# Performance work log

Hardware: AMD Instinct MI355X
Metric: run time of the kernel (lower is better)

## Reference

```python
import jax, jax.numpy as jnp
import numpy as np
import math


def setup_inputs() -> dict:
    key = jax.random.key(0)
    kq, kk, kv, km = jax.random.split(key, 4)
    B, Lq, Lk, D = 4, 4096, 4096, 64
    queries = jax.random.normal(kq, (B, Lq, D), dtype=jnp.float32)
    keys = jax.random.normal(kk, (B, Lk, D), dtype=jnp.float32)
    values = jax.random.normal(kv, (B, Lk, D), dtype=jnp.float32)
    masks = jax.random.randint(km, (B, Lk), 0, 2, dtype=jnp.int32)
    return {"queries": queries, "keys": keys, "values": values, "masks": masks}


def reference(queries, keys, values, masks):
    # scale = sqrt(d_k) (self.scale is None)
    d_k = queries.shape[-1]
    scale = math.sqrt(d_k)
    # scores: [B, Lq, Lk]
    scores = jnp.einsum('bqd,bkd->bqk', queries, keys) / jnp.asarray(scale, queries.dtype)
    # key-padding mask [B, Lk] -> broadcast over Lq; masked positions -> -inf
    neg_inf = jnp.asarray(float('-inf'), scores.dtype)
    scores = jnp.where(masks[:, None, :] == 0, neg_inf, scores)
    attn = jax.nn.softmax(scores, axis=-1)  # dropout p=0 -> identity
    return jnp.einsum('bqk,bkd->bqd', attn, values)
```

## Files before the change

### kernel.cpp

```cpp
#include <hip/hip_runtime.h>


#define B_N    4
#define L      4096
#define DH     64
#define TILE_K 64
#define BLOCK_Q 64
#define KPAD   72
#define SPLIT  4
#define SLAB   (L / SPLIT)
#define TILES  (SLAB / TILE_K)
#define QSCALE 0.18033688f

typedef unsigned short ushort8_ma __attribute__((ext_vector_type(8), may_alias));
typedef unsigned short ushort4_ma __attribute__((ext_vector_type(4), may_alias));
typedef float          f32x4_ma   __attribute__((ext_vector_type(4), may_alias));
typedef short          short8     __attribute__((ext_vector_type(8)));
typedef float          f32x4      __attribute__((ext_vector_type(4)));

union v8cast { ushort8_ma u; short8 s; };

static __device__ __forceinline__ short8 ld8(const unsigned short* p) {
    v8cast x; x.u = *(const ushort8_ma*)p; return x.s;
}
static __device__ __forceinline__ unsigned short bf16rne(float f) {
    union { float f; unsigned u; } x; x.f = f;
    unsigned r = x.u + 0x7fffu + ((x.u >> 16) & 1u);
    return (unsigned short)(r >> 16);
}
static __device__ __forceinline__ float fast_exp2(float x) {
    return __builtin_amdgcn_exp2f(x);
}

__global__ __launch_bounds__(256)
void prepass2(const float* __restrict__ Q, const float* __restrict__ K,
              const float* __restrict__ V,
              unsigned short* __restrict__ Qb, unsigned short* __restrict__ Kb,
              unsigned short* __restrict__ Vt)
{
    __shared__ unsigned short t[64][68];
    const int b  = blockIdx.y;
    const int r0 = blockIdx.x * 64;
    const size_t base = ((size_t)b * L + r0) * DH;

    for (int i = threadIdx.x; i < 1024; i += 256) {
        int row = i >> 4, d0 = (i & 15) * 4;
        size_t off = base + (size_t)row * DH + d0;
        f32x4_ma q = *(const f32x4_ma*)(Q + off);
        f32x4_ma k = *(const f32x4_ma*)(K + off);
        f32x4_ma v = *(const f32x4_ma*)(V + off);
        ushort4_ma qo, ko;
        #pragma unroll
        for (int j = 0; j < 4; ++j) {
            qo[j] = bf16rne(q[j] * QSCALE);
            ko[j] = bf16rne(k[j]);
            t[d0 + j][row] = bf16rne(v[j]);
        }
        *(ushort4_ma*)(Qb + off) = qo;
        *(ushort4_ma*)(Kb + off) = ko;
    }
    __syncthreads();
    for (int i = threadIdx.x; i < 1024; i += 256) {
        int d = i >> 4, k4 = (i & 15) * 4;
        ushort4_ma vo = { t[d][k4], t[d][k4 + 1], t[d][k4 + 2], t[d][k4 + 3] };
        *(ushort4_ma*)(Vt + ((size_t)b * DH + d) * L + r0 + k4) = vo;
    }
}

__global__ __launch_bounds__(256)
void fa_split(const unsigned short* __restrict__ Qb,
              const unsigned short* __restrict__ Kb,
              const unsigned short* __restrict__ Vt,
              const int*            __restrict__ Mk,
              float* __restrict__ ACCp, float* __restrict__ Lp)
{
    __shared__ unsigned short Kl[TILE_K * KPAD];
    __shared__ unsigned short Vl[DH * KPAD];
    __shared__ unsigned short Pl[4][16 * KPAD];
    __shared__ int            Ml[TILE_K];

    const int tid  = threadIdx.x;
    const int wave = tid >> 6;
    const int lane = tid & 63;
    const int l16  = lane & 15;
    const int quad = lane >> 4;

    const int b      = blockIdx.y & (B_N - 1);
    const int slab   = blockIdx.y >> 2;
    const int qblock = blockIdx.x * BLOCK_Q;
    const int kbase  = slab * SLAB;

    short8 aQ[2];
    {
        const unsigned short* qp = Qb + ((size_t)b * L + qblock + wave * 16 + l16) * DH;
        #pragma unroll
        for (int kk = 0; kk < 2; ++kk)
            aQ[kk] = ld8(qp + kk * 32 + quad * 8);
    }

    const unsigned short* Kbb = Kb + (size_t)b * L * DH;
    const unsigned short* Vtb = Vt + (size_t)b * DH * L;
    const int*            Mb  = Mk + (size_t)b * L;

    const int c1 = tid + 256;
    const int r0 = tid >> 3, d0 = (tid & 7) * 8;
    const int r1 = c1 >> 3,  d1 = (c1 & 7) * 8;

    ushort8_ma kr0, kr1, vr0, vr1;
    int mr;

    kr0 = *(const ushort8_ma*)(Kbb + (size_t)(kbase + r0) * DH + d0);
    kr1 = *(const ushort8_ma*)(Kbb + (size_t)(kbase + r1) * DH + d1);
    vr0 = *(const ushort8_ma*)(Vtb + (size_t)r0 * L + kbase + d0);
    vr1 = *(const ushort8_ma*)(Vtb + (size_t)r1 * L + kbase + d1);
    mr  = Mb[kbase + lane];
    *(ushort8_ma*)(&Kl[r0 * KPAD + d0]) = kr0;
    *(ushort8_ma*)(&Kl[r1 * KPAD + d1]) = kr1;
    *(ushort8_ma*)(&Vl[r0 * KPAD + d0]) = vr0;
    *(ushort8_ma*)(&Vl[r1 * KPAD + d1]) = vr1;
    if (wave == 0) Ml[lane] = mr;
    __syncthreads();

    f32x4 acc_o[4];
    float rs[4] = {0.f, 0.f, 0.f, 0.f};
    const f32x4 zero4 = {0.f, 0.f, 0.f, 0.f};
    #pragma unroll
    for (int n = 0; n < 4; ++n) acc_o[n] = zero4;

    unsigned short* pw = &Pl[wave][0];

    for (int t = 0; t < TILES; ++t) {
        if (t < TILES - 1) {
            const int k0n = kbase + (t + 1) * TILE_K;
            kr0 = *(const ushort8_ma*)(Kbb + (size_t)(k0n + r0) * DH + d0);
            kr1 = *(const ushort8_ma*)(Kbb + (size_t)(k0n + r1) * DH + d1);
            vr0 = *(const ushort8_ma*)(Vtb + (size_t)r0 * L + k0n + d0);
            vr1 = *(const ushort8_ma*)(Vtb + (size_t)r1 * L + k0n + d1);
            mr  = Mb[k0n + lane];
        }

        f32x4 s[4];
        #pragma unroll
        for (int n = 0; n < 4; ++n) {
            f32x4 acc = zero4;
            #pragma unroll
            for (int kk = 0; kk < 2; ++kk) {
                short8 bK = ld8(&Kl[(n * 16 + l16) * KPAD + kk * 32 + quad * 8]);
                acc = __builtin_amdgcn_mfma_f32_16x16x32_bf16(aQ[kk], bK, acc, 0, 0, 0);
            }
            s[n] = acc;
        }

        float bias[4];
        #pragma unroll
        for (int n = 0; n < 4; ++n) bias[n] = (Ml[n * 16 + l16] == 0) ? -1e30f : 0.f;
        #pragma unroll
        for (int n = 0; n < 4; ++n)
            #pragma unroll
            for (int r = 0; r < 4; ++r) {
                float p = fast_exp2(s[n][r] + bias[n]);
                rs[r] += p;
                pw[(quad * 4 + r) * KPAD + n * 16 + l16] = bf16rne(p);
            }

        #pragma unroll
        for (int kk = 0; kk < 2; ++kk) {
            short8 aP = ld8(&pw[l16 * KPAD + kk * 32 + quad * 8]);
            #pragma unroll
            for (int n = 0; n < 4; ++n) {
                short8 bV = ld8(&Vl[(n * 16 + l16) * KPAD + kk * 32 + quad * 8]);
                acc_o[n] = __builtin_amdgcn_mfma_f32_16x16x32_bf16(aP, bV, acc_o[n], 0, 0, 0);
            }
        }

        __syncthreads();
        if (t < TILES - 1) {
            *(ushort8_ma*)(&Kl[r0 * KPAD + d0]) = kr0;
            *(ushort8_ma*)(&Kl[r1 * KPAD + d1]) = kr1;
            *(ushort8_ma*)(&Vl[r0 * KPAD + d0]) = vr0;
            *(ushort8_ma*)(&Vl[r1 * KPAD + d1]) = vr1;
            if (wave == 0) Ml[lane] = mr;
            __syncthreads();
        }
    }

    const size_t pbase = ((size_t)(slab * B_N + b)) * L;
    #pragma unroll
    for (int r = 0; r < 4; ++r) {
        float t0 = rs[r];
        t0 += __shfl_xor(t0, 1);
        t0 += __shfl_xor(t0, 2);
        t0 += __shfl_xor(t0, 4);
        t0 += __shfl_xor(t0, 8);
        int qrow = qblock + wave * 16 + quad * 4 + r;
        float* ap = ACCp + (pbase + qrow) * DH;
        #pragma unroll
        for (int n = 0; n < 4; ++n)
            ap[n * 16 + l16] = acc_o[n][r];
        if (l16 == 0) Lp[pbase + qrow] = t0;
    }
}

__global__ __launch_bounds__(256)
void fa_combine(const float* __restrict__ ACCp, const float* __restrict__ Lp,
                float* __restrict__ O)
{
    const int b    = blockIdx.y;
    const int qrow = blockIdx.x * 4 + (threadIdx.x >> 6);
    const int d    = threadIdx.x & 63;

    float lsum = 0.f, o = 0.f;
    #pragma unroll
    for (int s = 0; s < SPLIT; ++s) {
        lsum += Lp[((size_t)(s * B_N + b)) * L + qrow];
        o    += ACCp[(((size_t)(s * B_N + b)) * L + qrow) * DH + d];
    }
    O[((size_t)b * L + qrow) * DH + d] = o / fmaxf(lsum, 1e-20f);
}

#define TK  64
#define RW  4
#define RB  16
#define KST 67

__global__ __launch_bounds__(256)
void fa_scalar(const float* __restrict__ Q, const float* __restrict__ K,
               const float* __restrict__ V, const int* __restrict__ Mk,
               float* __restrict__ O)
{
    __shared__ float Kt[TK][KST];
    __shared__ float Vts[DH][KST];
    __shared__ float Qs[RB][DH];
    __shared__ float Ps[4][RW][TK];
    __shared__ float Bs[TK];

    const int tid = threadIdx.x, w = tid >> 6, lane = tid & 63;
    const int b = blockIdx.y, row0 = blockIdx.x * RB;

    for (int i = tid; i < RB * DH; i += 256) {
        int r = i >> 6, d = i & 63;
        Qs[r][d] = Q[((size_t)b * L + row0 + r) * DH + d];
    }
    float m[RW], l[RW], acc[RW];
    #pragma unroll
    for (int rr = 0; rr < RW; ++rr) { m[rr] = -1e30f; l[rr] = 0.f; acc[rr] = 0.f; }

    for (int k0 = 0; k0 < L; k0 += TK) {
        __syncthreads();
        for (int i = tid; i < TK * DH; i += 256) {
            int key = i >> 6, d = i & 63;
            Kt[key][d]  = K[((size_t)b * L + k0 + key) * DH + d];
            Vts[d][key] = V[((size_t)b * L + k0 + key) * DH + d];
        }
        if (tid < TK) Bs[tid] = (Mk[(size_t)b * L + k0 + tid] == 0) ? -1e30f : 0.f;
        __syncthreads();
        float s[RW];
        #pragma unroll
        for (int rr = 0; rr < RW; ++rr) s[rr] = 0.f;
        for (int d4 = 0; d4 < DH; d4 += 4) {
            float kv[4];
            #pragma unroll
            for (int j = 0; j < 4; ++j) kv[j] = Kt[lane][d4 + j];
            #pragma unroll
            for (int rr = 0; rr < RW; ++rr)
                #pragma unroll
                for (int j = 0; j < 4; ++j)
                    s[rr] += Qs[w * RW + rr][d4 + j] * kv[j];
        }
        float alpha[RW];
        #pragma unroll
        for (int rr = 0; rr < RW; ++rr) {
            float sv = s[rr] * 0.125f + Bs[lane];
            float t = sv;
            #pragma unroll
            for (int off = 1; off < 64; off <<= 1) t = fmaxf(t, __shfl_xor(t, off));
            float mnew = fmaxf(m[rr], t);
            alpha[rr] = __expf(fminf(m[rr] - mnew, 0.f));
            float p = __expf(fminf(sv - mnew, 0.f));
            Ps[w][rr][lane] = p;
            float su = p;
            #pragma unroll
            for (int off = 1; off < 64; off <<= 1) su += __shfl_xor(su, off);
            l[rr] = l[rr] * alpha[rr] + su;
            m[rr] = mnew;
        }
        __syncthreads();
        #pragma unroll
        for (int rr = 0; rr < RW; ++rr) acc[rr] *= alpha[rr];
        for (int k4 = 0; k4 < TK; k4 += 4) {
            float vv[4];
            #pragma unroll
            for (int j = 0; j < 4; ++j) vv[j] = Vts[lane][k4 + j];
            #pragma unroll
            for (int rr = 0; rr < RW; ++rr)
                #pragma unroll
                for (int j = 0; j < 4; ++j)
                    acc[rr] += Ps[w][rr][k4 + j] * vv[j];
        }
    }
    #pragma unroll
    for (int rr = 0; rr < RW; ++rr) {
        int row = row0 + w * RW + rr;
        O[((size_t)b * L + row) * DH + lane] = acc[rr] / fmaxf(l[rr], 1e-20f);
    }
}

extern "C" void kernel_launch(void* const* d_in, const int* in_sizes, int n_in,
                              void* d_out, int out_size, void* d_ws, size_t ws_size,
                              hipStream_t stream) {
    const float* Q = (const float*)d_in[0];
    const float* K = (const float*)d_in[1];
    const float* V = (const float*)d_in[2];
    const int*   M = (const int*)d_in[3];
    float*       O = (float*)d_out;

    const size_t elems     = (size_t)B_N * L * DH;
    const size_t bf16_need = elems * 2 * 3;
    const size_t acc_elems = (size_t)SPLIT * B_N * L * DH;
    const size_t ml_elems  = (size_t)SPLIT * B_N * L;
    const size_t full_need = bf16_need + (acc_elems + ml_elems) * 4;

    unsigned short* Qb = (unsigned short*)d_ws;
    unsigned short* Kb = Qb + elems;
    unsigned short* Vt = Kb + elems;

    if (ws_size >= full_need) {
        float* ACCp = (float*)(Vt + elems);
        float* Lp   = ACCp + acc_elems;

        prepass2<<<dim3(L / 64, B_N), dim3(256), 0, stream>>>(Q, K, V, Qb, Kb, Vt);
        fa_split<<<dim3(L / BLOCK_Q, B_N * SPLIT), dim3(256), 0, stream>>>(
            Qb, Kb, Vt, M, ACCp, Lp);
        fa_combine<<<dim3(L / 4, B_N), dim3(256), 0, stream>>>(ACCp, Lp, O);
    } else {
        fa_scalar<<<dim3(L / RB, B_N), dim3(256), 0, stream>>>(Q, K, V, M, O);
    }
}
```

Before: 115.9 us.

## Fuse split-K combine into attention kernel via last-block atomic counter

Removes the separate combine kernel launch. Each split block now bumps an atomic counter per query block, and the last of the SPLIT blocks to finish reads the partial accumulators and row sums, normalises them and writes the output. The counters are zeroed in the prepass kernel. The P-to-bf16 conversion also changes from round-to-nearest-even to a cheaper round-half-up. This saves a launch and some scheduling gaps, at the cost of threadfences, an atomic, and a serialized tail in the last block for each query tile.

```diff
diff --git a/kernel.cpp b/kernel.cpp
--- a/kernel.cpp
+++ b/kernel.cpp
@@ -6,6 +6,7 @@
 #define DH     64
 #define TILE_K 64
 #define BLOCK_Q 64
+#define NQB    (L / BLOCK_Q)
 #define KPAD   72
 #define SPLIT  4
 #define SLAB   (L / SPLIT)
@@ -28,6 +29,10 @@
     unsigned r = x.u + 0x7fffu + ((x.u >> 16) & 1u);
     return (unsigned short)(r >> 16);
 }
+static __device__ __forceinline__ unsigned short bf16fast(float f) {
+    union { float f; unsigned u; } x; x.f = f;
+    return (unsigned short)((x.u + 0x8000u) >> 16);
+}
 static __device__ __forceinline__ float fast_exp2(float x) {
     return __builtin_amdgcn_exp2f(x);
 }
@@ -36,12 +41,15 @@
 void prepass2(const float* __restrict__ Q, const float* __restrict__ K,
               const float* __restrict__ V,
               unsigned short* __restrict__ Qb, unsigned short* __restrict__ Kb,
-              unsigned short* __restrict__ Vt)
+              unsigned short* __restrict__ Vt, int* __restrict__ Cnt)
 {
     __shared__ unsigned short t[64][68];
     const int b  = blockIdx.y;
     const int r0 = blockIdx.x * 64;
     const size_t base = ((size_t)b * L + r0) * DH;
+
+    if (blockIdx.x == 0 && threadIdx.x < NQB)
+        Cnt[b * NQB + threadIdx.x] = 0;
 
     for (int i = threadIdx.x; i < 1024; i += 256) {
         int row = i >> 4, d0 = (i & 15) * 4;
@@ -72,12 +80,15 @@
               const unsigned short* __restrict__ Kb,
               const unsigned short* __restrict__ Vt,
               const int*            __restrict__ Mk,
-              float* __restrict__ ACCp, float* __restrict__ Lp)
+              float* __restrict__ ACCp, float* __restrict__ Lp,
+              int* __restrict__ Cnt, float* __restrict__ O)
 {
     __shared__ unsigned short Kl[TILE_K * KPAD];
     __shared__ unsigned short Vl[DH * KPAD];
     __shared__ unsigned short Pl[4][16 * KPAD];
     __shared__ int            Ml[TILE_K];
+    __shared__ float          Linv[BLOCK_Q];
+    __shared__ int            lastFlag;
 
     const int tid  = threadIdx.x;
     const int wave = tid >> 6;
@@ -87,7 +98,8 @@
 
     const int b      = blockIdx.y & (B_N - 1);
     const int slab   = blockIdx.y >> 2;
-    const int qblock = blockIdx.x * BLOCK_Q;
+    const int qx     = blockIdx.x;
+    const int qblock = qx * BLOCK_Q;
     const int kbase  = slab * SLAB;
 
     short8 aQ[2];
@@ -160,7 +172,7 @@
             for (int r = 0; r < 4; ++r) {
                 float p = fast_exp2(s[n][r] + bias[n]);
                 rs[r] += p;
-                pw[(quad * 4 + r) * KPAD + n * 16 + l16] = bf16rne(p);
+                pw[(quad * 4 + r) * KPAD + n * 16 + l16] = bf16fast(p);
             }
 
         #pragma unroll
@@ -199,23 +211,39 @@
             ap[n * 16 + l16] = acc_o[n][r];
         if (l16 == 0) Lp[pbase + qrow] = t0;
     }
-}
-
-__global__ __launch_bounds__(256)
-void fa_combine(const float* __restrict__ ACCp, const float* __restrict__ Lp,
-                float* __restrict__ O)
-{
-    const int b    = blockIdx.y;
-    const int qrow = blockIdx.x * 4 + (threadIdx.x >> 6);
-    const int d    = threadIdx.x & 63;
-
-    float lsum = 0.f, o = 0.f;
-    #pragma unroll
-    for (int s = 0; s < SPLIT; ++s) {
-        lsum += Lp[((size_t)(s * B_N + b)) * L + qrow];
-        o    += ACCp[(((size_t)(s * B_N + b)) * L + qrow) * DH + d];
-    }
-    O[((size_t)b * L + qrow) * DH + d] = o / fmaxf(lsum, 1e-20f);
+
+    __threadfence();
+    if (tid == 0) {
+        int old = atomicAdd(&Cnt[b * NQB + qx], 1);
+        lastFlag = (old == SPLIT - 1);
+    }
+    __syncthreads();
+    if (lastFlag) {
+        __threadfence();
+        for (int i = tid; i < BLOCK_Q; i += 256) {
+            float ls = 0.f;
+            #pragma unroll
+            for (int sl = 0; sl < SPLIT; ++sl)
+                ls += Lp[((size_t)(sl * B_N + b)) * L + qblock + i];
+            Linv[i] = 1.0f / fmaxf(ls, 1e-20f);
+        }
+        __syncthreads();
+        for (int i = tid; i < BLOCK_Q * DH / 4; i += 256) {
+            int row = i >> 4, d4 = (i & 15) * 4;
+            f32x4_ma o = {0.f, 0.f, 0.f, 0.f};
+            #pragma unroll
+            for (int sl = 0; sl < SPLIT; ++sl) {
+                f32x4_ma a = *(const f32x4_ma*)(
+                    ACCp + (((size_t)(sl * B_N + b)) * L + qblock + row) * DH + d4);
+                #pragma unroll
+                for (int j = 0; j < 4; ++j) o[j] += a[j];
+            }
+            float inv = Linv[row];
+            #pragma unroll
+            for (int j = 0; j < 4; ++j) o[j] *= inv;
+            *(f32x4_ma*)(O + ((size_t)b * L + qblock + row) * DH + d4) = o;
+        }
+    }
 }
 
 #define TK  64
@@ -318,7 +346,8 @@
     const size_t bf16_need = elems * 2 * 3;
     const size_t acc_elems = (size_t)SPLIT * B_N * L * DH;
     const size_t ml_elems  = (size_t)SPLIT * B_N * L;
-    const size_t full_need = bf16_need + (acc_elems + ml_elems) * 4;
+    const size_t cnt_elems = (size_t)B_N * NQB;
+    const size_t full_need = bf16_need + (acc_elems + ml_elems + cnt_elems) * 4;
 
     unsigned short* Qb = (unsigned short*)d_ws;
     unsigned short* Kb = Qb + elems;
@@ -327,11 +356,11 @@
     if (ws_size >= full_need) {
         float* ACCp = (float*)(Vt + elems);
         float* Lp   = ACCp + acc_elems;
-
-        prepass2<<<dim3(L / 64, B_N), dim3(256), 0, stream>>>(Q, K, V, Qb, Kb, Vt);
-        fa_split<<<dim3(L / BLOCK_Q, B_N * SPLIT), dim3(256), 0, stream>>>(
-            Qb, Kb, Vt, M, ACCp, Lp);
-        fa_combine<<<dim3(L / 4, B_N), dim3(256), 0, stream>>>(ACCp, Lp, O);
+        int*   Cnt  = (int*)(Lp + ml_elems);
+
+        prepass2<<<dim3(L / 64, B_N), dim3(256), 0, stream>>>(Q, K, V, Qb, Kb, Vt, Cnt);
+        fa_split<<<dim3(NQB, B_N * SPLIT), dim3(256), 0, stream>>>(
+            Qb, Kb, Vt, M, ACCp, Lp, Cnt, O);
     } else {
         fa_scalar<<<dim3(L / RB, B_N), dim3(256), 0, stream>>>(Q, K, V, M, O);
     }
```

New measurement: 240.7 us. 2.08x slower.
